# Performance work log

Measured on AMD Instinct MI355X. Metric: run time of the kernel, lower is better.

## Reference

```python
import jax, jax.numpy as jnp
import numpy as np

N = 30000
E = 960000
F_IN = 16
NH1 = 36
NH2 = 36
KH = 8
IN_POOL = 2
OUT_POOL = 2
NUM_CLASSES = 10
RATIO = 0.1
EPS = 1e-5


def cheb_conv(x, src, dst, valid, W, b):
    """PyG ChebConv with sym normalization, lambda_max=2 -> L_hat = -D^-1/2 A D^-1/2.
    W: [K, in, out], valid: float mask [E] for (soft-)deleted edges."""
    n = x.shape[0]
    deg = jax.ops.segment_sum(valid, src, num_segments=n)
    dinv = jnp.where(deg > 0, jax.lax.rsqrt(deg), 0.0)
    norm = dinv[src] * dinv[dst] * valid  # [E]

    def prop(h):  # L_hat @ h
        return -jax.ops.segment_sum(norm[:, None] * h[src], dst, num_segments=n)

    k_hops = W.shape[0]
    tx0 = x
    out = tx0 @ W[0]
    if k_hops > 1:
        tx1 = prop(tx0)
        out = out + tx1 @ W[1]
        for kk in range(2, k_hops):
            tx2 = 2.0 * prop(tx1) - tx0
            out = out + tx2 @ W[kk]
            tx0, tx1 = tx1, tx2
    return out + b


def batch_norm(x, gamma, beta):
    mu = jnp.mean(x, axis=0)
    var = jnp.var(x, axis=0)
    return (x - mu) * jax.lax.rsqrt(var + EPS) * gamma + beta


def setup_inputs() -> dict:
    key = jax.random.key(0)
    ks = jax.random.split(key, 20)
    rn = lambda k, s: jax.random.normal(k, s, dtype=jnp.float32) * 0.1
    x = jax.random.normal(ks[0], (N, F_IN), dtype=jnp.float32)
    edge_index = jax.random.randint(ks[1], (2, E), 0, N, dtype=jnp.int32)
    return {
        "x": x,
        "edge_index": edge_index,
        "W1": rn(ks[2], (KH, F_IN, NH1)), "b1": jnp.zeros((NH1,), jnp.float32),
        "W2": rn(ks[3], (KH, NH1, NH2)), "b2": jnp.zeros((NH2,), jnp.float32),
        "g1": jnp.ones((NH1,), jnp.float32), "be1": jnp.zeros((NH1,), jnp.float32),
        "g2": jnp.ones((NH2,), jnp.float32), "be2": jnp.zeros((NH2,), jnp.float32),
        "Wc": rn(ks[4], (1, NH1, IN_POOL)), "bc": jnp.zeros((IN_POOL,), jnp.float32),
        "pool_w": rn(ks[5], (IN_POOL,)),
        "Wp": rn(ks[6], (KH, IN_POOL, OUT_POOL)), "bp": jnp.zeros((OUT_POOL,), jnp.float32),
        "W3": rn(ks[7], (1, NH1 + NH2 + OUT_POOL, NUM_CLASSES)),
        "b3": jnp.zeros((NUM_CLASSES,), jnp.float32),
    }


def reference(x, edge_index, W1, b1, W2, b2, g1, be1, g2, be2, Wc, bc, pool_w, Wp, bp, W3, b3):
    src, dst = edge_index[0], edge_index[1]
    valid = jnp.ones((src.shape[0],), jnp.float32)

    x1 = batch_norm(jax.nn.relu(cheb_conv(x, src, dst, valid, W1, b1)), g1, be1)
    x2 = batch_norm(jax.nn.relu(cheb_conv(x1, src, dst, valid, W2, b2)), g2, be2)
    xc = cheb_conv(x1, src, dst, valid, Wc, bc)

    # TopKPooling(ratio=0.1)
    score = jnp.tanh(xc @ pool_w / jnp.linalg.norm(pool_w))  # [N]
    k = int(np.ceil(RATIO * x.shape[0]))
    _, perm = jax.lax.top_k(score, k)
    xp1 = xc[perm] * score[perm][:, None]
    new_idx = jnp.full((x.shape[0],), -1, jnp.int32).at[perm].set(jnp.arange(k, dtype=jnp.int32))
    vs, vd = new_idx[src], new_idx[dst]
    valid_p = ((vs >= 0) & (vd >= 0)).astype(jnp.float32)
    src_p = jnp.where(vs >= 0, vs, 0)
    dst_p = jnp.where(vd >= 0, vd, 0)

    xp2 = cheb_conv(xp1, src_p, dst_p, valid_p, Wp, bp)  # [k, OUT_POOL]

    # nearest-neighbor unpooling using last-2 feature columns as 2D positions
    pos = x[:, -2:]              # [N, 2]
    pos_p = pos[perm]            # [k, 2]
    d2 = jnp.sum((pos[:, None, :] - pos_p[None, :, :]) ** 2, axis=-1)  # [N, k]
    nearest = jnp.argmin(d2, axis=1)
    x3u = xp2[nearest]           # [N, OUT_POOL]

    h = jnp.concatenate((x1, x2, x3u), axis=1)
    return cheb_conv(h, src, dst, valid, W3, b3)
```

## Files before the change

### kernel.cpp

```cpp
#include <hip/hip_runtime.h>
#include <cstdint>

constexpr int NN   = 30000;
constexpr int NE   = 960000;
constexpr int FIN  = 16;
constexpr int H1   = 36;
constexpr int H2   = 36;
constexpr int KHOP = 8;
constexpr int KSEL = 3000;
constexpr int PCAP = 32768;
constexpr int NCHUNK = 12;
constexpr int CHUNK = KSEL / NCHUNK;
constexpr int NB_H = 32;
constexpr int EPB  = (NE + NB_H - 1) / NB_H;
constexpr float EPSV = 1e-5f;

#define TPB 256

static inline int nb(long long t) { return (int)((t + TPB - 1) / TPB); }

__global__ void k_dinv2(const int* __restrict__ cnt, float* __restrict__ dinv, int n) {
    int i = blockIdx.x * blockDim.x + threadIdx.x;
    if (i < n) { int v = cnt[i]; dinv[i] = v > 0 ? rsqrtf((float)v) : 0.0f; }
}

__global__ __launch_bounds__(1024)
void k_hist(const int* __restrict__ src, const int* __restrict__ dst,
            int* __restrict__ partials, int* __restrict__ rank) {
    __shared__ int hist[NN];
    for (int j = threadIdx.x; j < NN; j += 1024) hist[j] = 0;
    __syncthreads();
    int b = blockIdx.x;
    int e0 = b * EPB, e1 = min(NE, e0 + EPB);
    if (blockIdx.y == 0) {
        for (int e = e0 + (int)threadIdx.x; e < e1; e += 1024)
            atomicAdd(&hist[src[e]], 1);
    } else {
        for (int e = e0 + (int)threadIdx.x; e < e1; e += 1024)
            rank[e] = atomicAdd(&hist[dst[e]], 1);
    }
    __syncthreads();
    int* P = partials + ((size_t)blockIdx.y * NB_H + b) * NN;
    for (int j = threadIdx.x; j < NN; j += 1024) P[j] = hist[j];
}

__global__ void k_red(int* __restrict__ partials, float* __restrict__ dinv,
                      int* __restrict__ cnt_dst) {
    int j = blockIdx.x * blockDim.x + threadIdx.x;
    if (j >= NN) return;
    const int* Ps = partials;
    int s = 0;
#pragma unroll
    for (int b = 0; b < NB_H; ++b) s += Ps[(size_t)b * NN + j];
    dinv[j] = s > 0 ? rsqrtf((float)s) : 0.0f;
    int* Pd = partials + (size_t)NB_H * NN;
    int run = 0;
#pragma unroll
    for (int b = 0; b < NB_H; ++b) {
        int t = Pd[(size_t)b * NN + j];
        Pd[(size_t)b * NN + j] = run;
        run += t;
    }
    cnt_dst[j] = run;
}

__device__ __forceinline__ int block_scan_excl_1024(int val, int& total) {
    __shared__ int wsum[16];
    int tid = threadIdx.x, lane = tid & 63, wv = tid >> 6;
    int v = val;
#pragma unroll
    for (int off = 1; off < 64; off <<= 1) {
        int t = __shfl_up(v, off, 64);
        if (lane >= off) v += t;
    }
    __syncthreads();
    if (lane == 63) wsum[wv] = v;
    __syncthreads();
    if (tid < 16) {
        int w = wsum[tid];
#pragma unroll
        for (int off = 1; off < 16; off <<= 1) {
            int t = __shfl_up(w, off, 64);
            if (tid >= off) w += t;
        }
        wsum[tid] = w;
    }
    __syncthreads();
    int base = (wv > 0) ? wsum[wv - 1] : 0;
    total = wsum[15];
    return base + v - val;
}

__global__ void k_scan(const int* __restrict__ cnt, int* __restrict__ rowstart, int n) {
    __shared__ int run;
    if (threadIdx.x == 0) run = 0;
    __syncthreads();
    for (int base = 0; base < n; base += 1024) {
        int i = base + threadIdx.x;
        int v = (i < n) ? cnt[i] : 0;
        int tot; int ex = block_scan_excl_1024(v, tot);
        int r = run;
        if (i < n) rowstart[i] = r + ex;
        __syncthreads();
        if (threadIdx.x == 0) run += tot;
        __syncthreads();
    }
    if (threadIdx.x == 0) rowstart[n] = run;
}

__global__ void k_fill3(const int* __restrict__ src, const int* __restrict__ dst,
                        const int* __restrict__ rank, const float* __restrict__ dinv,
                        const int* __restrict__ rowstart, const int* __restrict__ Pd_excl,
                        int2* __restrict__ csr, int E) {
    int e = blockIdx.x * blockDim.x + threadIdx.x;
    if (e >= E) return;
    int s = src[e], d = dst[e];
    int b = e / EPB;
    int pos = rowstart[d] + Pd_excl[(size_t)b * NN + d] + rank[e];
    float w = -dinv[s] * dinv[d];
    csr[pos] = make_int2(s, __float_as_int(w));
}

template<int F, int O>
__global__ void k_gemm_init(const float* __restrict__ in, const float* __restrict__ W,
                            const float* __restrict__ b, float* __restrict__ acc, int n) {
    __shared__ float sW[F * O];
    for (int i = threadIdx.x; i < F * O; i += blockDim.x) sW[i] = W[i];
    __syncthreads();
    int t = blockIdx.x * blockDim.x + threadIdx.x;
    if (t >= n * O) return;
    int node = t / O, o = t - node * O;
    const float* r = &in[node * F];
    float s = b[o];
#pragma unroll
    for (int f = 0; f < F; ++f) s = fmaf(r[f], sW[f * O + o], s);
    acc[t] = s;
}

template<int F, int O, int BN>
__global__ __launch_bounds__(BN * F / 4)
void k_prop_gemm(const int* __restrict__ rowstart, const int2* __restrict__ csr,
                 const float* __restrict__ h, const float* __restrict__ t0,
                 const float* __restrict__ W, float* __restrict__ tout,
                 float* __restrict__ acc, int n, int first) {
    constexpr int QF = F / 4;
    constexpr int NT = BN * QF;
    __shared__ float sT[BN * F];
    __shared__ float sW[F * O];
    const int tid = threadIdx.x;
    for (int i = tid; i < F * O; i += NT) sW[i] = W[i];
    const int nl = tid / QF, q = tid - nl * QF;
    const int node = blockIdx.x * BN + nl;
    if (node < n) {
        const float4* __restrict__ h4 = (const float4*)h;
        float4 p = {0.f, 0.f, 0.f, 0.f};
        int e0 = rowstart[node], e1 = rowstart[node + 1];
        int e = e0;
        for (; e + 3 < e1; e += 4) {
            int2 ea = csr[e];
            int2 eb = csr[e + 1];
            int2 ec = csr[e + 2];
            int2 ed = csr[e + 3];
            float4 ha = h4[ea.x * QF + q];
            float4 hb = h4[eb.x * QF + q];
            float4 hc = h4[ec.x * QF + q];
            float4 hd = h4[ed.x * QF + q];
            float wa = __int_as_float(ea.y), wb = __int_as_float(eb.y);
            float wc = __int_as_float(ec.y), wd = __int_as_float(ed.y);
            p.x = fmaf(wa, ha.x, p.x); p.y = fmaf(wa, ha.y, p.y);
            p.z = fmaf(wa, ha.z, p.z); p.w = fmaf(wa, ha.w, p.w);
            p.x = fmaf(wb, hb.x, p.x); p.y = fmaf(wb, hb.y, p.y);
            p.z = fmaf(wb, hb.z, p.z); p.w = fmaf(wb, hb.w, p.w);
            p.x = fmaf(wc, hc.x, p.x); p.y = fmaf(wc, hc.y, p.y);
            p.z = fmaf(wc, hc.z, p.z); p.w = fmaf(wc, hc.w, p.w);
            p.x = fmaf(wd, hd.x, p.x); p.y = fmaf(wd, hd.y, p.y);
            p.z = fmaf(wd, hd.z, p.z); p.w = fmaf(wd, hd.w, p.w);
        }
        for (; e < e1; ++e) {
            int2 ew = csr[e];
            float w = __int_as_float(ew.y);
            float4 hv = h4[ew.x * QF + q];
            p.x = fmaf(w, hv.x, p.x); p.y = fmaf(w, hv.y, p.y);
            p.z = fmaf(w, hv.z, p.z); p.w = fmaf(w, hv.w, p.w);
        }
        if (!first) {
            float4 tv = ((const float4*)t0)[node * QF + q];
            p.x = 2.f * p.x - tv.x; p.y = 2.f * p.y - tv.y;
            p.z = 2.f * p.z - tv.z; p.w = 2.f * p.w - tv.w;
        }
        ((float4*)tout)[node * QF + q] = p;
        sT[nl * F + 4 * q + 0] = p.x; sT[nl * F + 4 * q + 1] = p.y;
        sT[nl * F + 4 * q + 2] = p.z; sT[nl * F + 4 * q + 3] = p.w;
    }
    __syncthreads();
    for (int idx = tid; idx < BN * O; idx += NT) {
        int nl2 = idx / O, o = idx - nl2 * O;
        int gn = blockIdx.x * BN + nl2;
        if (gn >= n) break;
        float s = 0.f;
#pragma unroll
        for (int f = 0; f < F; ++f) s = fmaf(sT[nl2 * F + f], sW[f * O + o], s);
        acc[gn * O + o] += s;
    }
}

template<int C>
__global__ void k_colstats(const float* __restrict__ a, float* __restrict__ stats, int n) {
    __shared__ float s1[C], s2[C];
    for (int i = threadIdx.x; i < C; i += blockDim.x) { s1[i] = 0.f; s2[i] = 0.f; }
    __syncthreads();
    int total = n * C, stride = gridDim.x * blockDim.x;
    for (int t = blockIdx.x * blockDim.x + threadIdx.x; t < total; t += stride) {
        float v = fmaxf(a[t], 0.f); int c = t % C;
        atomicAdd(&s1[c], v); atomicAdd(&s2[c], v * v);
    }
    __syncthreads();
    for (int i = threadIdx.x; i < C; i += blockDim.x) {
        atomicAdd(&stats[i], s1[i]); atomicAdd(&stats[C + i], s2[i]);
    }
}

template<int C>
__global__ void k_bn(const float* __restrict__ a, const float* __restrict__ stats,
                     const float* __restrict__ g, const float* __restrict__ be,
                     float* __restrict__ o, int n) {
    int t = blockIdx.x * blockDim.x + threadIdx.x;
    if (t >= n * C) return;
    int c = t % C;
    float mu = stats[c] / n;
    float var = stats[C + c] / n - mu * mu;
    float v = fmaxf(a[t], 0.f);
    o[t] = (v - mu) * rsqrtf(var + EPSV) * g[c] + be[c];
}

__global__ void k_xc_score(const float* __restrict__ x1, const float* __restrict__ Wc,
                           const float* __restrict__ bc, const float* __restrict__ pw,
                           float* __restrict__ xc, float* __restrict__ score,
                           unsigned* __restrict__ key, int n) {
    int i = blockIdx.x * blockDim.x + threadIdx.x;
    if (i >= n) return;
    const float* r = &x1[i * H1];
    float a = bc[0], b = bc[1];
#pragma unroll
    for (int f = 0; f < H1; ++f) { float v = r[f]; a = fmaf(v, Wc[f * 2], a); b = fmaf(v, Wc[f * 2 + 1], b); }
    xc[i * 2] = a; xc[i * 2 + 1] = b;
    float w0 = pw[0], w1 = pw[1];
    float s = tanhf((a * w0 + b * w1) / sqrtf(w0 * w0 + w1 * w1));
    score[i] = s;
    unsigned u = __float_as_uint(s);
    key[i] = (u & 0x80000000u) ? ~u : (u | 0x80000000u);
}

__global__ void k_h16(const unsigned* __restrict__ key, int* __restrict__ gh, int n) {
    int i = blockIdx.x * blockDim.x + threadIdx.x;
    if (i < n) atomicAdd(&gh[key[i] >> 16], 1);
}

__global__ void k_h16b(const unsigned* __restrict__ key, const unsigned* __restrict__ pB,
                       int* __restrict__ gh, int n) {
    unsigned B = *pB;
    int i = blockIdx.x * blockDim.x + threadIdx.x;
    if (i < n && (key[i] >> 16) == B) atomicAdd(&gh[key[i] & 0xFFFFu], 1);
}

__global__ __launch_bounds__(1024)
void k_scanhist(const int* __restrict__ hist, const int* __restrict__ kin, int kdef,
                const unsigned* __restrict__ prevBin, unsigned* __restrict__ outT,
                int* __restrict__ outRem) {
    __shared__ int cs[1024];
    __shared__ int sC, sAbove;
    const int tid = threadIdx.x;
    int k = kin ? *kin : kdef;
    int s = 0;
    int base = tid * 64;
#pragma unroll 8
    for (int j = 0; j < 64; ++j) s += hist[base + j];
    cs[tid] = s;
    __syncthreads();
    int rsum = cs[1023 - tid];
    int tot; int ex = block_scan_excl_1024(rsum, tot);
    int c = 1023 - tid;
    if (ex < k && ex + cs[c] >= k) { sC = c; sAbove = ex; }
    __syncthreads();
    if (tid < 64) {
        int bin = sC * 64 + 63 - tid;
        int val = hist[bin];
        int incl = val;
#pragma unroll
        for (int off = 1; off < 64; off <<= 1) {
            int t2 = __shfl_up(incl, off, 64);
            if (tid >= off) incl += t2;
        }
        int above2 = sAbove + (incl - val);
        if (above2 < k && above2 + val >= k) {
            if (prevBin) *outT = ((*prevBin) << 16) | (unsigned)bin;
            else         *outT = (unsigned)bin;
            *outRem = k - above2;
        }
    }
}

__global__ __launch_bounds__(1024)
void k_selcnt(const unsigned* __restrict__ key, const unsigned* __restrict__ pT,
              int* __restrict__ bgt, int* __restrict__ beq, int n) {
    __shared__ int sgt, seq;
    if (threadIdx.x == 0) { sgt = 0; seq = 0; }
    __syncthreads();
    unsigned T = *pT;
    int i = blockIdx.x * 1024 + threadIdx.x;
    if (i < n) {
        unsigned kk = key[i];
        if (kk > T) atomicAdd(&sgt, 1);
        else if (kk == T) atomicAdd(&seq, 1);
    }
    __syncthreads();
    if (threadIdx.x == 0) { bgt[blockIdx.x] = sgt; beq[blockIdx.x] = seq; }
}

__global__ void k_seloff(const int* __restrict__ bgt, const int* __restrict__ beq,
                         const int* __restrict__ pR, int* __restrict__ eqoff,
                         int* __restrict__ soff, int nblk) {
    int t = threadIdx.x;
    int g = (t < nblk) ? bgt[t] : 0;
    int q = (t < nblk) ? beq[t] : 0;
    int gi = g, qi = q;
#pragma unroll
    for (int off = 1; off < 64; off <<= 1) {
        int a = __shfl_up(gi, off, 64);
        int b = __shfl_up(qi, off, 64);
        if (t >= off) { gi += a; qi += b; }
    }
    int qex = qi - q;
    int r = *pR;
    int eqsel = min(max(r - qex, 0), q);
    int scnt = g + eqsel;
    int si = scnt;
#pragma unroll
    for (int off = 1; off < 64; off <<= 1) {
        int a = __shfl_up(si, off, 64);
        if (t >= off) si += a;
    }
    if (t < nblk) { eqoff[t] = qex; soff[t] = si - scnt; }
}

__global__ __launch_bounds__(1024)
void k_selfill(const unsigned* __restrict__ key, const unsigned* __restrict__ pT,
               const int* __restrict__ pR, const int* __restrict__ eqoff,
               const int* __restrict__ soff, int* __restrict__ nidx,
               int* __restrict__ sel, int n) {
    unsigned T = *pT; int r = *pR;
    int b = blockIdx.x;
    int i = b * 1024 + threadIdx.x;
    unsigned kk = (i < n) ? key[i] : 0u;
    int eq = (i < n && kk == T) ? 1 : 0;
    int gt = (i < n && kk > T) ? 1 : 0;
    int eq_tot; int eq_ex = block_scan_excl_1024(eq, eq_tot);
    int sf = gt | (eq & (((eqoff[b] + eq_ex) < r) ? 1 : 0));
    int s_tot; int s_ex = block_scan_excl_1024(sf, s_tot);
    if (i < n) {
        if (sf) { int slot = soff[b] + s_ex; nidx[i] = slot; sel[slot] = i; }
        else nidx[i] = -1;
    }
}

__global__ void k_plen(const int* __restrict__ m_rowstart, const int2* __restrict__ m_csr,
                       const int* __restrict__ nidx, const int* __restrict__ sel,
                       int* __restrict__ pcnt, int* __restrict__ lens) {
    int wid = (blockIdx.x * blockDim.x + threadIdx.x) >> 6;
    int lane = threadIdx.x & 63;
    if (wid >= KSEL) return;
    int node = sel[wid];
    int e0 = m_rowstart[node], e1 = m_rowstart[node + 1];
    int cnt = 0;
    for (int e = e0 + lane; e < e1; e += 64) {
        int vs = nidx[m_csr[e].x];
        if (vs >= 0) { ++cnt; atomicAdd(&pcnt[vs], 1); }
    }
#pragma unroll
    for (int off = 32; off; off >>= 1) cnt += __shfl_down(cnt, off, 64);
    if (lane == 0) lens[wid] = cnt;
}

__global__ void k_pfill(const int* __restrict__ m_rowstart, const int2* __restrict__ m_csr,
                        const int* __restrict__ nidx, const int* __restrict__ sel,
                        const float* __restrict__ dinvp, const int* __restrict__ prs,
                        int2* __restrict__ gcsr) {
    int wid = (blockIdx.x * blockDim.x + threadIdx.x) >> 6;
    int lane = threadIdx.x & 63;
    if (wid >= KSEL) return;
    int node = sel[wid];
    int e0 = m_rowstart[node], e1 = m_rowstart[node + 1];
    float dd = dinvp[wid];
    int pos = prs[wid];
    for (int base = e0; base < e1; base += 64) {
        int e = base + lane;
        int vs = -1;
        if (e < e1) vs = nidx[m_csr[e].x];
        bool valid = vs >= 0;
        unsigned long long mask = __ballot(valid);
        if (valid) {
            int myoff = __popcll(mask & ((1ull << lane) - 1ull));
            float w = -dinvp[vs] * dd;
            gcsr[pos + myoff] = make_int2(vs, __float_as_int(w));
        }
        pos += __popcll(mask);
    }
}

__global__ __launch_bounds__(1024)
void k_pooled4(const int* __restrict__ prs_g, const int2* __restrict__ gcsr,
               const int* __restrict__ sel, const float* __restrict__ xc,
               const float* __restrict__ score, const float* __restrict__ x,
               const float* __restrict__ Wp, const float* __restrict__ bp,
               float* __restrict__ pacc_out, float* __restrict__ selpos) {
    __shared__ float bufA[2 * KSEL];
    __shared__ float bufB[2 * KSEL];
    __shared__ int   prs[KSEL + 1];
    const int tid = threadIdx.x, NT = 1024;

    for (int j = tid; j <= KSEL; j += NT) prs[j] = prs_g[j];

    const float bp0 = bp[0], bp1 = bp[1];
    float accA[3], accB[3];
#pragma unroll
    for (int r = 0; r < 3; ++r) {
        int j = tid + r * NT;
        accA[r] = 0.f; accB[r] = 0.f;
        if (j < KSEL) {
            int i = sel[j];
            float s = score[i];
            float a = xc[2 * i] * s, b = xc[2 * i + 1] * s;
            bufA[2 * j] = a; bufA[2 * j + 1] = b;
            accA[r] = bp0 + a * Wp[0] + b * Wp[2];
            accB[r] = bp1 + a * Wp[1] + b * Wp[3];
            selpos[2 * j] = x[i * FIN + 14];
            selpos[2 * j + 1] = x[i * FIN + 15];
        }
    }
    __syncthreads();

    for (int k = 1; k < KHOP; ++k) {
        float* rb = (k & 1) ? bufA : bufB;
        float* wb = (k & 1) ? bufB : bufA;
        float w0 = Wp[k * 4 + 0], w1 = Wp[k * 4 + 1];
        float w2 = Wp[k * 4 + 2], w3 = Wp[k * 4 + 3];
#pragma unroll
        for (int r = 0; r < 3; ++r) {
            int j = tid + r * NT;
            if (j < KSEL) {
                float pa = 0.f, pb = 0.f;
                int e0 = prs[j], e1 = prs[j + 1];
                for (int e = e0; e < e1; ++e) {
                    int2 ew = gcsr[e];
                    float w = __int_as_float(ew.y);
                    pa = fmaf(w, rb[2 * ew.x], pa);
                    pb = fmaf(w, rb[2 * ew.x + 1], pb);
                }
                if (k >= 2) {
                    pa = 2.f * pa - wb[2 * j];
                    pb = 2.f * pb - wb[2 * j + 1];
                }
                wb[2 * j] = pa; wb[2 * j + 1] = pb;
                accA[r] = fmaf(pa, w0, fmaf(pb, w2, accA[r]));
                accB[r] = fmaf(pa, w1, fmaf(pb, w3, accB[r]));
            }
        }
        __syncthreads();
    }

#pragma unroll
    for (int r = 0; r < 3; ++r) {
        int j = tid + r * NT;
        if (j < KSEL) {
            pacc_out[2 * j] = accA[r];
            pacc_out[2 * j + 1] = accB[r];
        }
    }
}

__global__ void k_near_part(const float* __restrict__ x, const float* __restrict__ selpos,
                            unsigned long long* __restrict__ best, int n) {
    __shared__ float2 sp[CHUNK];
    const int j0 = blockIdx.y * CHUNK;
    for (int j = threadIdx.x; j < CHUNK; j += blockDim.x)
        sp[j] = ((const float2*)selpos)[j0 + j];
    __syncthreads();
    int i = blockIdx.x * blockDim.x + threadIdx.x;
    if (i >= n) return;
    float px = x[i * FIN + 14], py = x[i * FIN + 15];
    float bd = 3.4e38f; int bj = 0;
#pragma unroll 2
    for (int j = 0; j < CHUNK; ++j) {
        float dx = px - sp[j].x, dy = py - sp[j].y;
        float d = fmaf(dx, dx, dy * dy);
        if (d < bd) { bd = d; bj = j0 + j; }
    }
    unsigned long long pk = ((unsigned long long)__float_as_uint(bd) << 32) | (unsigned)bj;
    atomicMin(&best[i], pk);
}

__global__ void k_final(const float* __restrict__ x1, const float* __restrict__ x2,
                        const float* __restrict__ xp2, const unsigned long long* __restrict__ best,
                        const float* __restrict__ W3, const float* __restrict__ b3,
                        float* __restrict__ o, int n) {
    __shared__ float sW[740], sb[10];
    for (int i = threadIdx.x; i < 740; i += blockDim.x) sW[i] = W3[i];
    if (threadIdx.x < 10) sb[threadIdx.x] = b3[threadIdx.x];
    __syncthreads();
    int t = blockIdx.x * blockDim.x + threadIdx.x;
    if (t >= n * 10) return;
    int i = t / 10, c = t - 10 * (t / 10);
    float s = sb[c];
    const float* r1 = &x1[i * H1];
#pragma unroll
    for (int f = 0; f < H1; ++f) s = fmaf(r1[f], sW[f * 10 + c], s);
    const float* r2 = &x2[i * H2];
#pragma unroll
    for (int f = 0; f < H2; ++f) s = fmaf(r2[f], sW[(H1 + f) * 10 + c], s);
    int m = (int)(best[i] & 0xFFFFFFFFull);
    s = fmaf(xp2[m * 2],     sW[720 + c], s);
    s = fmaf(xp2[m * 2 + 1], sW[730 + c], s);
    o[t] = s;
}

extern "C" void kernel_launch(void* const* d_in, const int* in_sizes, int n_in,
                              void* d_out, int out_size, void* d_ws, size_t ws_size,
                              hipStream_t stream) {
    const float* x   = (const float*)d_in[0];
    const int*   ei  = (const int*)d_in[1];
    const int*   src = ei;
    const int*   dst = ei + NE;
    const float* W1  = (const float*)d_in[2];
    const float* b1  = (const float*)d_in[3];
    const float* W2  = (const float*)d_in[4];
    const float* b2  = (const float*)d_in[5];
    const float* g1  = (const float*)d_in[6];
    const float* be1 = (const float*)d_in[7];
    const float* g2  = (const float*)d_in[8];
    const float* be2 = (const float*)d_in[9];
    const float* Wc  = (const float*)d_in[10];
    const float* bc  = (const float*)d_in[11];
    const float* pw  = (const float*)d_in[12];
    const float* Wp  = (const float*)d_in[13];
    const float* bp  = (const float*)d_in[14];
    const float* W3  = (const float*)d_in[15];
    const float* b3  = (const float*)d_in[16];
    float* out = (float*)d_out;

    char* w = (char*)d_ws;
    auto alloc = [&](size_t bytes) -> void* {
        void* p = (void*)w;
        w += (bytes + 255) & ~(size_t)255;
        return p;
    };
    int*   cnt_dst  = (int*)alloc(NN * 4);
    float* dinv     = (float*)alloc(NN * 4);
    int*   rowstart = (int*)alloc((NN + 1) * 4);
    int*   rank     = (int*)alloc((size_t)NE * 4);
    int2*  csr      = (int2*)alloc((size_t)NE * 8);
    float* B1    = (float*)alloc((size_t)NN * H1 * 4);
    float* B2    = (float*)alloc((size_t)NN * H1 * 4);
    float* B3    = (float*)alloc((size_t)NN * H1 * 4);
    float* acc   = (float*)alloc((size_t)NN * H1 * 4);
    float* x1    = (float*)alloc((size_t)NN * H1 * 4);
    float* x2    = (float*)alloc((size_t)NN * H2 * 4);
    float* xc    = (float*)alloc((size_t)NN * 2 * 4);
    float* score = (float*)alloc(NN * 4);
    float* stats = (float*)alloc(2 * H1 * 4);
    unsigned* key   = (unsigned*)alloc(NN * 4);
    int* nidx       = (int*)alloc(NN * 4);
    int* sel        = (int*)alloc(KSEL * 4);
    unsigned long long* best = (unsigned long long*)alloc(NN * 8);
    unsigned* Tptr  = (unsigned*)alloc(4);
    int* Rptr       = (int*)alloc(4);
    unsigned* BinPtr = (unsigned*)alloc(4);
    int* RemPtr     = (int*)alloc(4);
    int* gh         = (int*)alloc(2 * 65536 * 4);
    int* bgt        = (int*)alloc(64 * 4);
    int* beq        = (int*)alloc(64 * 4);
    int* eqoff      = (int*)alloc(64 * 4);
    int* soff       = (int*)alloc(64 * 4);
    int* pcnt       = (int*)alloc(KSEL * 4);
    int* lens       = (int*)alloc(KSEL * 4);
    int* prs        = (int*)alloc((KSEL + 1) * 4);
    float* dinvp    = (float*)alloc(KSEL * 4);
    int2* gcsr      = (int2*)alloc((size_t)PCAP * 8);
    float* pacc     = (float*)alloc(KSEL * 2 * 4);
    float* selpos   = (float*)alloc(KSEL * 2 * 4);

    int* partials = (int*)B1;

    const int NBK = (NN + 63) / 64;

    hipMemsetAsync(pcnt, 0, KSEL * 4, stream);
    hipMemsetAsync(best, 0xFF, NN * 8, stream);
    hipMemsetAsync(gh, 0, 2 * 65536 * 4, stream);

    {
        dim3 gh2(NB_H, 2);
        k_hist<<<gh2, 1024, 0, stream>>>(src, dst, partials, rank);
        k_red<<<nb(NN), TPB, 0, stream>>>(partials, dinv, cnt_dst);
        k_scan<<<1, 1024, 0, stream>>>(cnt_dst, rowstart, NN);
        k_fill3<<<nb(NE), TPB, 0, stream>>>(src, dst, rank, dinv, rowstart,
                                            partials + (size_t)NB_H * NN, csr, NE);
    }

    {
        k_gemm_init<FIN, H1><<<nb((long long)NN * H1), TPB, 0, stream>>>(x, W1, b1, acc, NN);
        float* rot[3] = {B1, B2, B3};
        k_prop_gemm<FIN, H1, 64><<<NBK, 64 * (FIN / 4), 0, stream>>>(
            rowstart, csr, x, nullptr, W1 + FIN * H1, B1, acc, NN, 1);
        const float* t_prev = x; const float* t_cur = B1;
        for (int kk = 2; kk < KHOP; ++kk) {
            float* o = rot[(kk - 1) % 3];
            k_prop_gemm<FIN, H1, 64><<<NBK, 64 * (FIN / 4), 0, stream>>>(
                rowstart, csr, t_cur, t_prev, W1 + kk * FIN * H1, o, acc, NN, 0);
            t_prev = t_cur; t_cur = o;
        }
        hipMemsetAsync(stats, 0, 2 * H1 * 4, stream);
        k_colstats<H1><<<120, TPB, 0, stream>>>(acc, stats, NN);
        k_bn<H1><<<nb((long long)NN * H1), TPB, 0, stream>>>(acc, stats, g1, be1, x1, NN);
    }

    {
        k_gemm_init<H1, H2><<<nb((long long)NN * H2), TPB, 0, stream>>>(x1, W2, b2, acc, NN);
        float* rot[3] = {B1, B2, B3};
        k_prop_gemm<H1, H2, 64><<<NBK, 64 * (H1 / 4), 0, stream>>>(
            rowstart, csr, x1, nullptr, W2 + H1 * H2, B1, acc, NN, 1);
        const float* t_prev = x1; const float* t_cur = B1;
        for (int kk = 2; kk < KHOP; ++kk) {
            float* o = rot[(kk - 1) % 3];
            k_prop_gemm<H1, H2, 64><<<NBK, 64 * (H1 / 4), 0, stream>>>(
                rowstart, csr, t_cur, t_prev, W2 + kk * H1 * H2, o, acc, NN, 0);
            t_prev = t_cur; t_cur = o;
        }
        hipMemsetAsync(stats, 0, 2 * H2 * 4, stream);
        k_colstats<H2><<<120, TPB, 0, stream>>>(acc, stats, NN);
        k_bn<H2><<<nb((long long)NN * H2), TPB, 0, stream>>>(acc, stats, g2, be2, x2, NN);
    }

    k_xc_score<<<nb(NN), TPB, 0, stream>>>(x1, Wc, bc, pw, xc, score, key, NN);

    k_h16<<<nb(NN), TPB, 0, stream>>>(key, gh, NN);
    k_scanhist<<<1, 1024, 0, stream>>>(gh, nullptr, KSEL, nullptr, BinPtr, RemPtr);
    k_h16b<<<nb(NN), TPB, 0, stream>>>(key, BinPtr, gh + 65536, NN);
    k_scanhist<<<1, 1024, 0, stream>>>(gh + 65536, RemPtr, 0, BinPtr, Tptr, Rptr);

    {
        const int SB = (NN + 1023) / 1024;
        k_selcnt<<<SB, 1024, 0, stream>>>(key, Tptr, bgt, beq, NN);
        k_seloff<<<1, 64, 0, stream>>>(bgt, beq, Rptr, eqoff, soff, SB);
        k_selfill<<<SB, 1024, 0, stream>>>(key, Tptr, Rptr, eqoff, soff, nidx, sel, NN);
    }

    {
        const int WPB = TPB / 64;
        const int GB = (KSEL + WPB - 1) / WPB;
        k_plen<<<GB, TPB, 0, stream>>>(rowstart, csr, nidx, sel, pcnt, lens);
        k_scan<<<1, 1024, 0, stream>>>(lens, prs, KSEL);
        k_dinv2<<<nb(KSEL), TPB, 0, stream>>>(pcnt, dinvp, KSEL);
        k_pfill<<<GB, TPB, 0, stream>>>(rowstart, csr, nidx, sel, dinvp, prs, gcsr);
    }

    k_pooled4<<<1, 1024, 0, stream>>>(prs, gcsr, sel, xc, score, x, Wp, bp, pacc, selpos);

    {
        dim3 g(nb(NN), NCHUNK);
        k_near_part<<<g, TPB, 0, stream>>>(x, selpos, best, NN);
    }
    k_final<<<nb((long long)NN * 10), TPB, 0, stream>>>(x1, x2, pacc, best, W3, b3, out, NN);
}
```

Measured before the change: 575.5 us.

## Compress CSR to 16-bit source indices and factor normalization out of edges

Each CSR entry shrinks from an int2 (source index plus precomputed weight) to a 16-bit source index. The per-edge weight is rebuilt in the propagation kernels as dinv[src], and the row is scaled by -dinv[dst] once at the end. This cuts CSR storage and read bandwidth by 4x across all 14 propagation passes, at the cost of an extra gather from the small, cache-resident dinv array. The histogram block count also doubles and the unroll pragmas in the reduction are dropped. A 16-bit index only holds because N=30000 fits in an unsigned short.

```diff
diff --git a/kernel.cpp b/kernel.cpp
--- a/kernel.cpp
+++ b/kernel.cpp
@@ -11,7 +11,7 @@
 constexpr int PCAP = 32768;
 constexpr int NCHUNK = 12;
 constexpr int CHUNK = KSEL / NCHUNK;
-constexpr int NB_H = 32;
+constexpr int NB_H = 64;
 constexpr int EPB  = (NE + NB_H - 1) / NB_H;
 constexpr float EPSV = 1e-5f;
 
@@ -50,12 +50,10 @@
     if (j >= NN) return;
     const int* Ps = partials;
     int s = 0;
-#pragma unroll
     for (int b = 0; b < NB_H; ++b) s += Ps[(size_t)b * NN + j];
     dinv[j] = s > 0 ? rsqrtf((float)s) : 0.0f;
     int* Pd = partials + (size_t)NB_H * NN;
     int run = 0;
-#pragma unroll
     for (int b = 0; b < NB_H; ++b) {
         int t = Pd[(size_t)b * NN + j];
         Pd[(size_t)b * NN + j] = run;
@@ -109,16 +107,15 @@
 }
 
 __global__ void k_fill3(const int* __restrict__ src, const int* __restrict__ dst,
-                        const int* __restrict__ rank, const float* __restrict__ dinv,
-                        const int* __restrict__ rowstart, const int* __restrict__ Pd_excl,
-                        int2* __restrict__ csr, int E) {
+                        const int* __restrict__ rank, const int* __restrict__ rowstart,
+                        const int* __restrict__ Pd_excl,
+                        unsigned short* __restrict__ csr16, int E) {
     int e = blockIdx.x * blockDim.x + threadIdx.x;
     if (e >= E) return;
     int s = src[e], d = dst[e];
     int b = e / EPB;
     int pos = rowstart[d] + Pd_excl[(size_t)b * NN + d] + rank[e];
-    float w = -dinv[s] * dinv[d];
-    csr[pos] = make_int2(s, __float_as_int(w));
+    csr16[pos] = (unsigned short)s;
 }
 
 template<int F, int O>
@@ -139,7 +136,8 @@
 
 template<int F, int O, int BN>
 __global__ __launch_bounds__(BN * F / 4)
-void k_prop_gemm(const int* __restrict__ rowstart, const int2* __restrict__ csr,
+void k_prop_gemm(const int* __restrict__ rowstart, const unsigned short* __restrict__ csr16,
+                 const float* __restrict__ dinv,
                  const float* __restrict__ h, const float* __restrict__ t0,
                  const float* __restrict__ W, float* __restrict__ tout,
                  float* __restrict__ acc, int n, int first) {
@@ -154,19 +152,19 @@
     if (node < n) {
         const float4* __restrict__ h4 = (const float4*)h;
         float4 p = {0.f, 0.f, 0.f, 0.f};
+        float dd = dinv[node];
         int e0 = rowstart[node], e1 = rowstart[node + 1];
         int e = e0;
         for (; e + 3 < e1; e += 4) {
-            int2 ea = csr[e];
-            int2 eb = csr[e + 1];
-            int2 ec = csr[e + 2];
-            int2 ed = csr[e + 3];
-            float4 ha = h4[ea.x * QF + q];
-            float4 hb = h4[eb.x * QF + q];
-            float4 hc = h4[ec.x * QF + q];
-            float4 hd = h4[ed.x * QF + q];
-            float wa = __int_as_float(ea.y), wb = __int_as_float(eb.y);
-            float wc = __int_as_float(ec.y), wd = __int_as_float(ed.y);
+            int sa = csr16[e];
+            int sb = csr16[e + 1];
+            int sc = csr16[e + 2];
+            int sd = csr16[e + 3];
+            float wa = dinv[sa], wb = dinv[sb], wc = dinv[sc], wd = dinv[sd];
+            float4 ha = h4[sa * QF + q];
+            float4 hb = h4[sb * QF + q];
+            float4 hc = h4[sc * QF + q];
+            float4 hd = h4[sd * QF + q];
             p.x = fmaf(wa, ha.x, p.x); p.y = fmaf(wa, ha.y, p.y);
             p.z = fmaf(wa, ha.z, p.z); p.w = fmaf(wa, ha.w, p.w);
             p.x = fmaf(wb, hb.x, p.x); p.y = fmaf(wb, hb.y, p.y);
@@ -177,12 +175,14 @@
             p.z = fmaf(wd, hd.z, p.z); p.w = fmaf(wd, hd.w, p.w);
         }
         for (; e < e1; ++e) {
-            int2 ew = csr[e];
-            float w = __int_as_float(ew.y);
-            float4 hv = h4[ew.x * QF + q];
+            int sa = csr16[e];
+            float w = dinv[sa];
+            float4 hv = h4[sa * QF + q];
             p.x = fmaf(w, hv.x, p.x); p.y = fmaf(w, hv.y, p.y);
             p.z = fmaf(w, hv.z, p.z); p.w = fmaf(w, hv.w, p.w);
         }
+        float ndd = -dd;
+        p.x *= ndd; p.y *= ndd; p.z *= ndd; p.w *= ndd;
         if (!first) {
             float4 tv = ((const float4*)t0)[node * QF + q];
             p.x = 2.f * p.x - tv.x; p.y = 2.f * p.y - tv.y;
@@ -363,7 +363,7 @@
     }
 }
 
-__global__ void k_plen(const int* __restrict__ m_rowstart, const int2* __restrict__ m_csr,
+__global__ void k_plen(const int* __restrict__ m_rowstart, const unsigned short* __restrict__ csr16,
                        const int* __restrict__ nidx, const int* __restrict__ sel,
                        int* __restrict__ pcnt, int* __restrict__ lens) {
     int wid = (blockIdx.x * blockDim.x + threadIdx.x) >> 6;
@@ -373,7 +373,7 @@
     int e0 = m_rowstart[node], e1 = m_rowstart[node + 1];
     int cnt = 0;
     for (int e = e0 + lane; e < e1; e += 64) {
-        int vs = nidx[m_csr[e].x];
+        int vs = nidx[csr16[e]];
         if (vs >= 0) { ++cnt; atomicAdd(&pcnt[vs], 1); }
     }
 #pragma unroll
@@ -381,7 +381,7 @@
     if (lane == 0) lens[wid] = cnt;
 }
 
-__global__ void k_pfill(const int* __restrict__ m_rowstart, const int2* __restrict__ m_csr,
+__global__ void k_pfill(const int* __restrict__ m_rowstart, const unsigned short* __restrict__ csr16,
                         const int* __restrict__ nidx, const int* __restrict__ sel,
                         const float* __restrict__ dinvp, const int* __restrict__ prs,
                         int2* __restrict__ gcsr) {
@@ -395,7 +395,7 @@
     for (int base = e0; base < e1; base += 64) {
         int e = base + lane;
         int vs = -1;
-        if (e < e1) vs = nidx[m_csr[e].x];
+        if (e < e1) vs = nidx[csr16[e]];
         bool valid = vs >= 0;
         unsigned long long mask = __ballot(valid);
         if (valid) {
@@ -557,7 +557,7 @@
     float* dinv     = (float*)alloc(NN * 4);
     int*   rowstart = (int*)alloc((NN + 1) * 4);
     int*   rank     = (int*)alloc((size_t)NE * 4);
-    int2*  csr      = (int2*)alloc((size_t)NE * 8);
+    unsigned short* csr16 = (unsigned short*)alloc((size_t)NE * 2);
     float* B1    = (float*)alloc((size_t)NN * H1 * 4);
     float* B2    = (float*)alloc((size_t)NN * H1 * 4);
     float* B3    = (float*)alloc((size_t)NN * H1 * 4);
@@ -601,20 +601,20 @@
         k_hist<<<gh2, 1024, 0, stream>>>(src, dst, partials, rank);
         k_red<<<nb(NN), TPB, 0, stream>>>(partials, dinv, cnt_dst);
         k_scan<<<1, 1024, 0, stream>>>(cnt_dst, rowstart, NN);
-        k_fill3<<<nb(NE), TPB, 0, stream>>>(src, dst, rank, dinv, rowstart,
-                                            partials + (size_t)NB_H * NN, csr, NE);
+        k_fill3<<<nb(NE), TPB, 0, stream>>>(src, dst, rank, rowstart,
+                                            partials + (size_t)NB_H * NN, csr16, NE);
     }
 
     {
         k_gemm_init<FIN, H1><<<nb((long long)NN * H1), TPB, 0, stream>>>(x, W1, b1, acc, NN);
         float* rot[3] = {B1, B2, B3};
         k_prop_gemm<FIN, H1, 64><<<NBK, 64 * (FIN / 4), 0, stream>>>(
-            rowstart, csr, x, nullptr, W1 + FIN * H1, B1, acc, NN, 1);
+            rowstart, csr16, dinv, x, nullptr, W1 + FIN * H1, B1, acc, NN, 1);
         const float* t_prev = x; const float* t_cur = B1;
         for (int kk = 2; kk < KHOP; ++kk) {
             float* o = rot[(kk - 1) % 3];
             k_prop_gemm<FIN, H1, 64><<<NBK, 64 * (FIN / 4), 0, stream>>>(
-                rowstart, csr, t_cur, t_prev, W1 + kk * FIN * H1, o, acc, NN, 0);
+                rowstart, csr16, dinv, t_cur, t_prev, W1 + kk * FIN * H1, o, acc, NN, 0);
             t_prev = t_cur; t_cur = o;
         }
         hipMemsetAsync(stats, 0, 2 * H1 * 4, stream);
@@ -626,12 +626,12 @@
         k_gemm_init<H1, H2><<<nb((long long)NN * H2), TPB, 0, stream>>>(x1, W2, b2, acc, NN);
         float* rot[3] = {B1, B2, B3};
         k_prop_gemm<H1, H2, 64><<<NBK, 64 * (H1 / 4), 0, stream>>>(
-            rowstart, csr, x1, nullptr, W2 + H1 * H2, B1, acc, NN, 1);
+            rowstart, csr16, dinv, x1, nullptr, W2 + H1 * H2, B1, acc, NN, 1);
         const float* t_prev = x1; const float* t_cur = B1;
         for (int kk = 2; kk < KHOP; ++kk) {
             float* o = rot[(kk - 1) % 3];
             k_prop_gemm<H1, H2, 64><<<NBK, 64 * (H1 / 4), 0, stream>>>(
-                rowstart, csr, t_cur, t_prev, W2 + kk * H1 * H2, o, acc, NN, 0);
+                rowstart, csr16, dinv, t_cur, t_prev, W2 + kk * H1 * H2, o, acc, NN, 0);
             t_prev = t_cur; t_cur = o;
         }
         hipMemsetAsync(stats, 0, 2 * H2 * 4, stream);
@@ -656,10 +656,10 @@
     {
         const int WPB = TPB / 64;
         const int GB = (KSEL + WPB - 1) / WPB;
-        k_plen<<<GB, TPB, 0, stream>>>(rowstart, csr, nidx, sel, pcnt, lens);
+        k_plen<<<GB, TPB, 0, stream>>>(rowstart, csr16, nidx, sel, pcnt, lens);
         k_scan<<<1, 1024, 0, stream>>>(lens, prs, KSEL);
         k_dinv2<<<nb(KSEL), TPB, 0, stream>>>(pcnt, dinvp, KSEL);
-        k_pfill<<<GB, TPB, 0, stream>>>(rowstart, csr, nidx, sel, dinvp, prs, gcsr);
+        k_pfill<<<GB, TPB, 0, stream>>>(rowstart, csr16, nidx, sel, dinvp, prs, gcsr);
     }
 
     k_pooled4<<<1, 1024, 0, stream>>>(prs, gcsr, sel, xc, score, x, Wp, bp, pacc, selpos);
```

Result: slower. 602.7 us (+4.7%).
